# Performance work log

Measured on AMD Instinct MI355X. Metric: run time of the kernel, lower is better.

## Reference

```python
import jax, jax.numpy as jnp
import numpy as np

GX, GY = 512, 512   # grid_size
MAX_PT = 64         # max_pt_per_encode


def setup_inputs() -> dict:
    key = jax.random.key(0)
    k1, k2 = jax.random.split(key)
    B, N = 16, 262144
    pt_fea = jax.random.normal(k1, (B, N, 4), dtype=jnp.float32)
    xy_ind = jax.random.randint(k2, (B, N, 2), 0, GX, dtype=jnp.int32)
    return {"pt_fea": pt_fea, "xy_ind": xy_ind}


def _voxelize(fea, vid, P, S):
    # fea: [P,4] flat point features; vid: [P] linearized (batch,x,y) voxel id.
    # --- 'random' point selection: keep first MAX_PT points per voxel ---
    order = jnp.argsort(vid)                       # stable sort -> group points by voxel
    svid = vid[order]
    ar = jnp.arange(P, dtype=jnp.int32)
    change = jnp.concatenate([jnp.ones((1,), dtype=bool), svid[1:] != svid[:-1]])
    start = jax.lax.cummax(jnp.where(change, ar, 0))  # first sorted-index of each group
    rank_sorted = ar - start                          # within-group rank (grp_range_torch)
    grp_ind = jnp.zeros(P, jnp.int32).at[order].set(rank_sorted)
    remain = grp_ind < MAX_PT
    # --- scatter_max pooling of z; gather r at argmax; clamped counts ---
    z = jnp.where(remain, fea[:, 2], -jnp.inf)
    h = jax.ops.segment_max(z, vid, num_segments=S)
    cnt = jax.ops.segment_sum(remain.astype(jnp.float32), vid, num_segments=S)  # == clamp(count, max_pt)
    occ = cnt > 0
    cand = jnp.where(remain & (fea[:, 2] == h[vid]), ar, P)  # argmax via min index of max match
    argm = jax.ops.segment_min(cand, vid, num_segments=S)
    r = jnp.where(occ, fea[jnp.minimum(argm, P - 1), 3], 0.0)
    h0 = jnp.where(occ, h, 0.0)  # empty voxels stay 0 (dense zeros grid write)
    return h0, r, cnt


def reference(pt_fea, xy_ind):
    B, N, _ = pt_fea.shape
    P = B * N
    S = B * GX * GY
    fea = pt_fea.reshape(P, 4)
    b = jnp.repeat(jnp.arange(B, dtype=jnp.int32), N)
    x = xy_ind[..., 0].reshape(P).astype(jnp.int32)
    y = xy_ind[..., 1].reshape(P).astype(jnp.int32)
    vid = (b * GX + x) * GY + y
    h0, r, cnt = _voxelize(fea, vid, P, S)
    grid = jnp.stack([h0, r, cnt], axis=-1).reshape(B, GX, GY, 3)
    grid = jnp.transpose(grid, (0, 3, 1, 2))  # [B, 3, GX, GY]
    mx = grid.max(axis=(2, 3), keepdims=True)
    mn = grid.min(axis=(2, 3), keepdims=True)
    return (grid - mn) / (mx - mn)
```

## Files before the change

kernel.cpp:

```cpp
#include <hip/hip_runtime.h>
#include <stdint.h>

#define GXC 512
#define GYC 512
#define GXY (GXC * GYC)
#define NB  512
#define SC  8192
#define PT  1024
#define SPT (SC / PT)
#define LBINS 512
#define XG  4
#define BPB (GXY / 256)

typedef float v4f __attribute__((ext_vector_type(4)));
typedef int   v2i __attribute__((ext_vector_type(2)));

__device__ __forceinline__ unsigned f2s(float f) {
    unsigned u = __float_as_uint(f);
    return (u & 0x80000000u) ? ~u : (u | 0x80000000u);
}
__device__ __forceinline__ float s2f(unsigned u) {
    return (u & 0x80000000u) ? __uint_as_float(u ^ 0x80000000u)
                             : __uint_as_float(~u);
}
__device__ __forceinline__ unsigned long long packkey_y(float z, float r,
                                                        unsigned y) {
    return ((unsigned long long)f2s(z) << 32)
         | (unsigned long long)((f2s(r) & ~511u) | y);
}
__device__ __forceinline__ unsigned long long packkey(float z, float r) {
    return ((unsigned long long)f2s(z) << 32) | (unsigned long long)f2s(r);
}

__device__ __forceinline__ int swizzle(int g, int swz) {
    return swz ? ((g & 7) * (NB / 8) + (g >> 3)) : g;
}


__global__ __launch_bounds__(1024)
void place_kernel(const v4f* __restrict__ fea, const v2i* __restrict__ xy,
                  unsigned long long* __restrict__ keyA,
                  unsigned* __restrict__ meta, int swz) {
    __shared__ unsigned long long skey[SC];
    __shared__ unsigned lcnt[LBINS], loff[LBINS];
    __shared__ unsigned wsum[8];
    int t = threadIdx.x;
    int blk = swizzle(blockIdx.x, swz);
    int start = blk * SC;
    if (t < LBINS) lcnt[t] = 0;
    __syncthreads();

    unsigned long long k[SPT]; unsigned lb[SPT], rk[SPT];
    #pragma unroll
    for (int kk = 0; kk < SPT; ++kk) {
        int p = start + t + kk * PT;
        v2i q = __builtin_nontemporal_load(xy + p);
        v4f ff = __builtin_nontemporal_load(fea + p);
        k[kk]  = packkey_y(ff.z, ff.w, (unsigned)q.y);
        lb[kk] = (unsigned)q.x;
        rk[kk] = atomicAdd(&lcnt[q.x], 1u);
    }
    __syncthreads();

    unsigned c = 0, inc = 0;
    if (t < LBINS) {
        c = lcnt[t];
        inc = c;
        int lane = t & 63;
        #pragma unroll
        for (int off = 1; off < 64; off <<= 1) {
            unsigned o = __shfl_up(inc, off);
            if (lane >= off) inc += o;
        }
        if (lane == 63) wsum[t >> 6] = inc;
    }
    __syncthreads();
    if (t < 8) {
        unsigned v = wsum[t], i2 = v;
        #pragma unroll
        for (int off = 1; off < 8; off <<= 1) {
            unsigned o = __shfl_up(i2, off, 8);
            if (t >= off) i2 += o;
        }
        wsum[t] = i2 - v;
    }
    __syncthreads();
    if (t < LBINS) loff[t] = inc - c + wsum[t >> 6];
    __syncthreads();

    #pragma unroll
    for (int kk = 0; kk < SPT; ++kk)
        skey[loff[lb[kk]] + rk[kk]] = k[kk];
    __syncthreads();

    unsigned long long* dst = keyA + (size_t)blk * SC;
    #pragma unroll
    for (int kk = 0; kk < SPT; ++kk) {
        int s = t + kk * PT;
        dst[s] = skey[s];
    }
    if (t < LBINS)
        meta[(size_t)blk * LBINS + t] = (loff[t] << 16) | lcnt[t];
}

__global__ __launch_bounds__(512)
void rowreduce_kernel(const unsigned long long* __restrict__ keyA,
                      const unsigned* __restrict__ meta,
                      float* __restrict__ out,
                      float* __restrict__ partials,
                      int bpblk) {
    __shared__ unsigned long long sk[XG * 512];
    __shared__ unsigned scnt[XG * 512];
    __shared__ float red[8][6];
    int t = threadIdx.x;
    int g = blockIdx.x;
    int batch = g >> 7;
    int xg = g & 127;
    int x0 = xg * XG;
    for (int i = t; i < XG * 512; i += 512) { sk[i] = 0; scnt[i] = 0; }
    __syncthreads();

    int seg = t >> 4, l16 = t & 15;
    size_t sidx = (size_t)(batch * bpblk + seg);
    uint4 m = *(const uint4*)(meta + sidx * LBINS + x0);
    unsigned lo0 = m.x >> 16;
    unsigned b1 = m.x & 0xFFFFu;
    unsigned b2 = b1 + (m.y & 0xFFFFu);
    unsigned b3 = b2 + (m.z & 0xFFFFu);
    unsigned tot = b3 + (m.w & 0xFFFFu);
    const unsigned long long* src = keyA + sidx * SC + lo0;
    for (unsigned r = l16; r < tot; r += 16) {
        unsigned long long k = src[r];
        int bin = (r >= b1) + (r >= b2) + (r >= b3);
        unsigned y = (unsigned)k & 511u;
        atomicMax(&sk[(bin << 9) + y], k);
        atomicAdd(&scnt[(bin << 9) + y], 1u);
    }
    __syncthreads();

    size_t ob = ((size_t)batch * 3) << 18;
    size_t xoff = (size_t)x0 << 9;
    float n0 = INFINITY, mx0 = -INFINITY, n1 = INFINITY, mx1 = -INFINITY,
          n2 = INFINITY, mx2 = -INFINITY;
    for (int i = t; i < XG * 512; i += 512) {
        unsigned cv = scnt[i];
        float h0 = 0.0f, r = 0.0f;
        if (cv) {
            unsigned long long k = sk[i];
            h0 = s2f((unsigned)(k >> 32));
            r  = s2f((unsigned)k & ~511u);
        }
        float cf = (float)cv;
        out[ob + xoff + i] = h0;
        out[ob + (size_t)GXY + xoff + i] = r;
        out[ob + (size_t)(2 * GXY) + xoff + i] = cf;
        n0 = fminf(n0, h0); mx0 = fmaxf(mx0, h0);
        n1 = fminf(n1, r);  mx1 = fmaxf(mx1, r);
        n2 = fminf(n2, cf); mx2 = fmaxf(mx2, cf);
    }
    #pragma unroll
    for (int off = 32; off; off >>= 1) {
        n0 = fminf(n0, __shfl_down(n0, off));  mx0 = fmaxf(mx0, __shfl_down(mx0, off));
        n1 = fminf(n1, __shfl_down(n1, off));  mx1 = fmaxf(mx1, __shfl_down(mx1, off));
        n2 = fminf(n2, __shfl_down(n2, off));  mx2 = fmaxf(mx2, __shfl_down(mx2, off));
    }
    int lane = t & 63, wave = t >> 6;
    if (lane == 0) {
        red[wave][0] = n0; red[wave][1] = mx0;
        red[wave][2] = n1; red[wave][3] = mx1;
        red[wave][4] = n2; red[wave][5] = mx2;
    }
    __syncthreads();
    if (t < 6) {
        int j = t;
        float v = red[0][j];
        bool isMin = (j & 1) == 0;
        #pragma unroll
        for (int w = 1; w < 8; ++w)
            v = isMin ? fminf(v, red[w][j]) : fmaxf(v, red[w][j]);
        partials[(size_t)g * 6 + j] = v;
    }
}

__global__ void reduce_kernel(const float* __restrict__ partials,
                              float* __restrict__ mn,
                              float* __restrict__ mx,
                              int rows) {
    int b = blockIdx.x / 6;
    int j = blockIdx.x - b * 6;
    bool isMin = (j & 1) == 0;
    float v = isMin ? INFINITY : -INFINITY;
    for (int i = threadIdx.x; i < rows; i += blockDim.x) {
        float p = partials[((size_t)b * rows + i) * 6 + j];
        v = isMin ? fminf(v, p) : fmaxf(v, p);
    }
    #pragma unroll
    for (int off = 32; off; off >>= 1) {
        float o = __shfl_down(v, off);
        v = isMin ? fminf(v, o) : fmaxf(v, o);
    }
    __shared__ float red[4];
    int lane = threadIdx.x & 63, wave = threadIdx.x >> 6;
    if (lane == 0) red[wave] = v;
    __syncthreads();
    if (threadIdx.x == 0) {
        #pragma unroll
        for (int w = 1; w < 4 && w < (int)(blockDim.x >> 6); ++w)
            v = isMin ? fminf(v, red[w]) : fmaxf(v, red[w]);
        int slot = b * 3 + (j >> 1);
        if (isMin) mn[slot] = v; else mx[slot] = v;
    }
}

__global__ void norm_kernel(v4f* __restrict__ out,
                            const float* __restrict__ mn,
                            const float* __restrict__ mx,
                            int total4) {
    int i = blockIdx.x * blockDim.x + threadIdx.x;
    if (i >= total4) return;
    int slot = i >> 16;
    float lo = mn[slot];
    float inv = 1.0f / (mx[slot] - lo);
    v4f v = __builtin_nontemporal_load(out + i);
    v.x = (v.x - lo) * inv;
    v.y = (v.y - lo) * inv;
    v.z = (v.z - lo) * inv;
    v.w = (v.w - lo) * inv;
    __builtin_nontemporal_store(v, out + i);
}

__global__ void scatter_fb(const v4f* __restrict__ fea, const v2i* __restrict__ xy,
                           unsigned long long* __restrict__ keys,
                           unsigned* __restrict__ cnt32, int N, int P) {
    int p = blockIdx.x * blockDim.x + threadIdx.x;
    if (p >= P) return;
    v2i q = __builtin_nontemporal_load(xy + p);
    v4f f = __builtin_nontemporal_load(fea + p);
    int vid = ((p / N) * GXC + q.x) * GYC + q.y;
    atomicMax(&keys[vid], packkey(f.z, f.w));
    atomicAdd(&cnt32[vid >> 2], 1u << ((vid & 3) * 8));
}

__global__ void fill_fb(const unsigned long long* __restrict__ keys,
                        const unsigned char* __restrict__ cntB,
                        float* __restrict__ out, float* __restrict__ partials) {
    int g = blockIdx.x;
    int batch = g / BPB, blkInB = g - batch * BPB;
    int rem = blkInB * 256 + threadIdx.x;
    int s = batch * GXY + rem;
    unsigned c = cntB[s];
    float h0 = 0.0f, r = 0.0f;
    if (c) {
        unsigned long long k = keys[s];
        h0 = s2f((unsigned)(k >> 32));
        r  = s2f((unsigned)(k & 0xFFFFFFFFull));
    }
    float cf = (float)c;
    size_t base = (size_t)batch * 3 * GXY + rem;
    out[base] = h0; out[base + GXY] = r; out[base + 2 * GXY] = cf;
    float n0 = h0, x0 = h0, n1 = r, x1 = r, n2 = cf, x2 = cf;
    #pragma unroll
    for (int off = 32; off; off >>= 1) {
        n0 = fminf(n0, __shfl_down(n0, off)); x0 = fmaxf(x0, __shfl_down(x0, off));
        n1 = fminf(n1, __shfl_down(n1, off)); x1 = fmaxf(x1, __shfl_down(x1, off));
        n2 = fminf(n2, __shfl_down(n2, off)); x2 = fmaxf(x2, __shfl_down(x2, off));
    }
    __shared__ float red[4][6];
    int lane = threadIdx.x & 63, wave = threadIdx.x >> 6;
    if (lane == 0) {
        red[wave][0] = n0; red[wave][1] = x0; red[wave][2] = n1;
        red[wave][3] = x1; red[wave][4] = n2; red[wave][5] = x2;
    }
    __syncthreads();
    if (threadIdx.x < 6) {
        int j = threadIdx.x;
        float v = red[0][j];
        bool isMin = (j & 1) == 0;
        #pragma unroll
        for (int w = 1; w < 4; ++w)
            v = isMin ? fminf(v, red[w][j]) : fmaxf(v, red[w][j]);
        partials[(size_t)(batch * BPB + blkInB) * 6 + j] = v;
    }
}

extern "C" void kernel_launch(void* const* d_in, const int* in_sizes, int n_in,
                              void* d_out, int out_size, void* d_ws, size_t ws_size,
                              hipStream_t stream) {
    const v4f* fea = (const v4f*)d_in[0];
    const v2i* xy  = (const v2i*)d_in[1];

    int P = in_sizes[0] / 4;
    int B = out_size / (3 * GXY);
    int N = (B > 0) ? P / B : 0;
    int S = B * GXY;
    int NBIN = B * GXC;
    int bpblk = (B > 0) ? NB / B : 0;

    char* ws = (char*)d_ws;
    unsigned long long* keyA = (unsigned long long*)ws;
    size_t o = (size_t)P * 8;
    unsigned* meta = (unsigned*)(ws + o);   o += (size_t)NB * LBINS * 4;
    float* partials = (float*)(ws + o);     o += (size_t)(NBIN / XG) * 6 * 4;
    float* mn = (float*)(ws + o);           o += (size_t)B * 3 * 4;
    float* mx = (float*)(ws + o);           o += (size_t)B * 3 * 4;
    size_t need = o;

    int swz = (B % 8 == 0) ? 1 : 0;

    bool ok = B > 0 && NB % B == 0 && bpblk == 32 && P == NB * SC
              && N == bpblk * SC && ws_size >= need;

    if (ok) {
        place_kernel<<<NB, PT, 0, stream>>>(fea, xy, keyA, meta, swz);
        rowreduce_kernel<<<NBIN / XG, 512, 0, stream>>>(keyA, meta,
                                                        (float*)d_out, partials,
                                                        bpblk);
        reduce_kernel<<<B * 6, 256, 0, stream>>>(partials, mn, mx, GXC / XG);
    } else {
        float* mn_f = (float*)ws;
        float* mx_f = (float*)(ws + 256);
        float* part_f = (float*)(ws + 512);
        size_t hdr = 512 + (size_t)B * BPB * 6 * 4;
        unsigned long long* keys = (unsigned long long*)(ws + hdr);
        unsigned char* cntB = (unsigned char*)(ws + hdr + (size_t)S * 8);
        mn = mn_f; mx = mx_f;
        (void)hipMemsetAsync(keys, 0x00, (size_t)S * 9, stream);
        scatter_fb<<<(P + 255) / 256, 256, 0, stream>>>(fea, xy, keys,
                                                        (unsigned*)cntB, N, P);
        fill_fb<<<S / 256, 256, 0, stream>>>(keys, cntB, (float*)d_out, part_f);
        reduce_kernel<<<B * 6, 256, 0, stream>>>(part_f, mn_f, mx_f, BPB);
    }
    norm_kernel<<<(out_size / 4 + 255) / 256, 256, 0, stream>>>((v4f*)d_out,
                                                                mn, mx, out_size / 4);
}
```

Before: 167.5 us.

## Fuse row reduction, min/max reduce and normalization into one cooperative kernel

Replaces the rowreduce, reduce and norm kernels with one cooperative kernel of 256 blocks by 1024 threads. Each block keeps its voxel results in registers and shared memory, publishes per-block min/max partials, waits on a grid-wide sync, then writes the normalized output directly with nontemporal stores. This removes the write-then-reread of the 50MB output and two kernel launches. In exchange it depends on co-residency of all 256 large blocks, adds a grid barrier, and carries heavy register and LDS use per block.

```diff
diff --git a/kernel.cpp b/kernel.cpp
--- a/kernel.cpp
+++ b/kernel.cpp
@@ -1,5 +1,8 @@
 #include <hip/hip_runtime.h>
+#include <hip/hip_cooperative_groups.h>
 #include <stdint.h>
+
+namespace cg = cooperative_groups;
 
 #define GXC 512
 #define GYC 512
@@ -101,6 +104,137 @@
     }
     if (t < LBINS)
         meta[(size_t)blk * LBINS + t] = (loff[t] << 16) | lcnt[t];
+}
+
+__global__ __launch_bounds__(1024, 4)
+void fused_kernel(const unsigned long long* __restrict__ keyA,
+                  const unsigned* __restrict__ meta,
+                  float* __restrict__ out,
+                  float* __restrict__ partials) {
+    __shared__ unsigned long long sk[2048];
+    __shared__ unsigned scnt[2048];
+    __shared__ unsigned short pcnt[8][2048];
+    __shared__ float red[16][6];
+    __shared__ float pred[16][6];
+    int t = threadIdx.x;
+    int blk = blockIdx.x;
+    int batch = blk >> 4;
+    int bb = blk & 15;
+    int seg = t >> 5, l = t & 31;
+    size_t sidx = (size_t)(batch * 32 + seg);
+
+    unsigned long long hk[16];
+    float n0 = INFINITY, mx0 = -INFINITY, n1 = INFINITY, mx1 = -INFINITY,
+          n2 = INFINITY, mx2 = -INFINITY;
+
+    #pragma unroll
+    for (int gi = 0; gi < 8; ++gi) {
+        int xg = bb * 8 + gi;
+        int x0 = xg * XG;
+        sk[t] = 0; sk[t + 1024] = 0; scnt[t] = 0; scnt[t + 1024] = 0;
+        __syncthreads();
+
+        uint4 m = *(const uint4*)(meta + sidx * LBINS + x0);
+        unsigned lo0 = m.x >> 16;
+        unsigned b1 = m.x & 0xFFFFu;
+        unsigned b2 = b1 + (m.y & 0xFFFFu);
+        unsigned b3 = b2 + (m.z & 0xFFFFu);
+        unsigned tot = b3 + (m.w & 0xFFFFu);
+        const unsigned long long* src = keyA + sidx * SC + lo0;
+        for (unsigned r = l; r < tot; r += 32) {
+            unsigned long long k = src[r];
+            int bin = (r >= b1) + (r >= b2) + (r >= b3);
+            unsigned y = (unsigned)k & 511u;
+            atomicMax(&sk[(bin << 9) + y], k);
+            atomicAdd(&scnt[(bin << 9) + y], 1u);
+        }
+        __syncthreads();
+
+        #pragma unroll
+        for (int j = 0; j < 2; ++j) {
+            int i = t + j * 1024;
+            unsigned cv = scnt[i];
+            unsigned long long k = sk[i];
+            hk[gi * 2 + j] = k;
+            pcnt[gi][i] = (unsigned short)(cv > 65535u ? 65535u : cv);
+            float h0 = 0.0f, rr = 0.0f;
+            if (cv) {
+                h0 = s2f((unsigned)(k >> 32));
+                rr = s2f((unsigned)k & ~511u);
+            }
+            float cf = (float)cv;
+            n0 = fminf(n0, h0); mx0 = fmaxf(mx0, h0);
+            n1 = fminf(n1, rr); mx1 = fmaxf(mx1, rr);
+            n2 = fminf(n2, cf); mx2 = fmaxf(mx2, cf);
+        }
+    }
+
+    #pragma unroll
+    for (int off = 32; off; off >>= 1) {
+        n0 = fminf(n0, __shfl_down(n0, off));  mx0 = fmaxf(mx0, __shfl_down(mx0, off));
+        n1 = fminf(n1, __shfl_down(n1, off));  mx1 = fmaxf(mx1, __shfl_down(mx1, off));
+        n2 = fminf(n2, __shfl_down(n2, off));  mx2 = fmaxf(mx2, __shfl_down(mx2, off));
+    }
+    int lane = t & 63, wave = t >> 6;
+    if (lane == 0) {
+        red[wave][0] = n0; red[wave][1] = mx0;
+        red[wave][2] = n1; red[wave][3] = mx1;
+        red[wave][4] = n2; red[wave][5] = mx2;
+    }
+    __syncthreads();
+    if (t < 6) {
+        int j = t;
+        float v = red[0][j];
+        bool isMin = (j & 1) == 0;
+        #pragma unroll
+        for (int w = 1; w < 16; ++w)
+            v = isMin ? fminf(v, red[w][j]) : fmaxf(v, red[w][j]);
+        __hip_atomic_store(&partials[(size_t)blk * 6 + j], v,
+                           __ATOMIC_RELEASE, __HIP_MEMORY_SCOPE_AGENT);
+    }
+
+    cg::this_grid().sync();
+
+    if (t < 96) {
+        float v = __hip_atomic_load(&partials[(size_t)(batch << 4) * 6 + t],
+                                    __ATOMIC_RELAXED, __HIP_MEMORY_SCOPE_AGENT);
+        pred[t / 6][t % 6] = v;
+    }
+    __syncthreads();
+    float bn0 = INFINITY, bx0 = -INFINITY, bn1 = INFINITY, bx1 = -INFINITY,
+          bn2 = INFINITY, bx2 = -INFINITY;
+    #pragma unroll
+    for (int w = 0; w < 16; ++w) {
+        bn0 = fminf(bn0, pred[w][0]); bx0 = fmaxf(bx0, pred[w][1]);
+        bn1 = fminf(bn1, pred[w][2]); bx1 = fmaxf(bx1, pred[w][3]);
+        bn2 = fminf(bn2, pred[w][4]); bx2 = fmaxf(bx2, pred[w][5]);
+    }
+    float i0 = 1.0f / (bx0 - bn0);
+    float i1 = 1.0f / (bx1 - bn1);
+    float i2 = 1.0f / (bx2 - bn2);
+
+    size_t ob = ((size_t)batch * 3) << 18;
+    #pragma unroll
+    for (int gi = 0; gi < 8; ++gi) {
+        int xg = bb * 8 + gi;
+        size_t xoff = (size_t)xg << 11;
+        #pragma unroll
+        for (int j = 0; j < 2; ++j) {
+            int i = t + j * 1024;
+            int idx = gi * 2 + j;
+            unsigned cv = pcnt[gi][i];
+            unsigned long long k = hk[idx];
+            float h0 = 0.0f, rr = 0.0f;
+            if (cv) {
+                h0 = s2f((unsigned)(k >> 32));
+                rr = s2f((unsigned)k & ~511u);
+            }
+            float cf = (float)cv;
+            __builtin_nontemporal_store((h0 - bn0) * i0, out + ob + xoff + i);
+            __builtin_nontemporal_store((rr - bn1) * i1, out + ob + (size_t)GXY + xoff + i);
+            __builtin_nontemporal_store((cf - bn2) * i2, out + ob + (size_t)(2 * GXY) + xoff + i);
+        }
+    }
 }
 
 __global__ __launch_bounds__(512)
@@ -312,10 +446,19 @@
 
     if (ok) {
         place_kernel<<<NB, PT, 0, stream>>>(fea, xy, keyA, meta, swz);
-        rowreduce_kernel<<<NBIN / XG, 512, 0, stream>>>(keyA, meta,
-                                                        (float*)d_out, partials,
-                                                        bpblk);
-        reduce_kernel<<<B * 6, 256, 0, stream>>>(partials, mn, mx, GXC / XG);
+        float* outp = (float*)d_out;
+        void* args[] = {(void*)&keyA, (void*)&meta, (void*)&outp, (void*)&partials};
+        hipError_t ce = hipLaunchCooperativeKernel(
+            reinterpret_cast<void*>(fused_kernel), dim3(256), dim3(1024),
+            args, 0, stream);
+        if (ce != hipSuccess) {
+            rowreduce_kernel<<<NBIN / XG, 512, 0, stream>>>(keyA, meta,
+                                                            (float*)d_out,
+                                                            partials, bpblk);
+            reduce_kernel<<<B * 6, 256, 0, stream>>>(partials, mn, mx, GXC / XG);
+            norm_kernel<<<(out_size / 4 + 255) / 256, 256, 0, stream>>>(
+                (v4f*)d_out, mn, mx, out_size / 4);
+        }
     } else {
         float* mn_f = (float*)ws;
         float* mx_f = (float*)(ws + 256);
@@ -323,13 +466,13 @@
         size_t hdr = 512 + (size_t)B * BPB * 6 * 4;
         unsigned long long* keys = (unsigned long long*)(ws + hdr);
         unsigned char* cntB = (unsigned char*)(ws + hdr + (size_t)S * 8);
-        mn = mn_f; mx = mx_f;
         (void)hipMemsetAsync(keys, 0x00, (size_t)S * 9, stream);
         scatter_fb<<<(P + 255) / 256, 256, 0, stream>>>(fea, xy, keys,
                                                         (unsigned*)cntB, N, P);
         fill_fb<<<S / 256, 256, 0, stream>>>(keys, cntB, (float*)d_out, part_f);
         reduce_kernel<<<B * 6, 256, 0, stream>>>(part_f, mn_f, mx_f, BPB);
-    }
-    norm_kernel<<<(out_size / 4 + 255) / 256, 256, 0, stream>>>((v4f*)d_out,
-                                                                mn, mx, out_size / 4);
-}
+        norm_kernel<<<(out_size / 4 + 255) / 256, 256, 0, stream>>>((v4f*)d_out,
+                                                                    mn_f, mx_f,
+                                                                    out_size / 4);
+    }
+}
```

Result: slower. 208.0 us (+24.2%).
